# Kernel optimization log

Hardware: AMD Instinct MI355X
Metric: run time of the kernel (lower is better)

## Reference

```python
import jax, jax.numpy as jnp
import numpy as np

EPS = 1e-12

def gcn_layer(x, W, row, col, vals, n_nodes):
    # support = x @ W ; out = relu(spmm(adj, support)) with adj in COO form
    support = x @ W                                  # [N, out]
    msgs = vals[:, None] * support[col]              # [E, out] gather
    agg = jax.ops.segment_sum(msgs, row, num_segments=n_nodes)
    return jax.nn.relu(agg)

def l2norm(x):
    return x / jnp.maximum(jnp.linalg.norm(x, axis=1, keepdims=True), EPS)

def setup_inputs() -> dict:
    key = jax.random.key(0)
    ks = jax.random.split(key, 16)
    N, D, A, Da, E = 20000, 1000, 1000, 100, 160000
    inp = {
        'emb_sr': jax.random.normal(ks[0], (N, D), jnp.float32) * 0.02,
        'emb_tg': jax.random.normal(ks[1], (N, D), jnp.float32) * 0.02,
        'attr_weight_sr': jax.random.uniform(ks[2], (N, A), jnp.float32),
        'attr_weight_tg': jax.random.uniform(ks[3], (N, A), jnp.float32),
        'row_sr': jax.random.randint(ks[4], (E,), 0, N, jnp.int32),
        'col_sr': jax.random.randint(ks[5], (E,), 0, N, jnp.int32),
        'vals_sr': jax.random.uniform(ks[6], (E,), jnp.float32),
        'row_tg': jax.random.randint(ks[7], (E,), 0, N, jnp.int32),
        'col_tg': jax.random.randint(ks[8], (E,), 0, N, jnp.int32),
        'vals_tg': jax.random.uniform(ks[9], (E,), jnp.float32),
        'W_s0': jax.random.normal(ks[10], (D, D), jnp.float32) * (1.0 / np.sqrt(D)),
        'W_s1': jax.random.normal(ks[11], (D, D), jnp.float32) * (1.0 / np.sqrt(D)),
        'W_a11': jax.random.normal(ks[12], (A, Da), jnp.float32) * (1.0 / np.sqrt(A)),
        'W_a12': jax.random.normal(ks[13], (A, Da), jnp.float32) * (1.0 / np.sqrt(A)),
        'W_a2': jax.random.normal(ks[14], (Da, Da), jnp.float32) * (1.0 / np.sqrt(Da)),
    }
    return inp

def reference(emb_sr, emb_tg, attr_weight_sr, attr_weight_tg,
              row_sr, col_sr, vals_sr, row_tg, col_tg, vals_tg,
              W_s0, W_s1, W_a11, W_a12, W_a2):
    N = emb_sr.shape[0]
    M = emb_tg.shape[0]
    # structural branch: 2 shared GCN layers over each graph
    sr = emb_sr
    tg = emb_tg
    for W in (W_s0, W_s1):
        sr = gcn_layer(sr, W, row_sr, col_sr, vals_sr, N)
        tg = gcn_layer(tg, W, row_tg, col_tg, vals_tg, M)
    sr = l2norm(sr)
    tg = l2norm(tg)
    # attribute branch
    sr_a = gcn_layer(attr_weight_sr, W_a11, row_sr, col_sr, vals_sr, N)
    sr_a = gcn_layer(sr_a, W_a2, row_sr, col_sr, vals_sr, N)
    tg_a = gcn_layer(attr_weight_tg, W_a12, row_tg, col_tg, vals_tg, M)
    tg_a = gcn_layer(tg_a, W_a2, row_tg, col_tg, vals_tg, M)
    return (sr, tg, sr_a, tg_a)
```

## Files before the change

### kernel.cpp

```cpp
#include <hip/hip_runtime.h>

#define N_NODES 20000
#define D_IN    1000
#define E_EDGES 160000
#define DA      100

#define MP   20096
#define DP   1024
#define DAP  128
#define MBLK 157
#define PEMAX (E_EDGES + 4 * N_NODES)

typedef __bf16 bf16x8 __attribute__((ext_vector_type(8)));
typedef float  f32x4  __attribute__((ext_vector_type(4)));

__device__ __forceinline__ short f2bf(float f) {
  unsigned u = __float_as_uint(f);
  return (short)((u + 0x7FFFu + ((u >> 16) & 1u)) >> 16);
}
__device__ __forceinline__ float bf2f(short s) {
  return __uint_as_float(((unsigned)(unsigned short)s) << 16);
}

#define GLDS16(g, l) __builtin_amdgcn_global_load_lds( \
    (const __attribute__((address_space(1))) void*)(g), \
    (__attribute__((address_space(3))) void*)(l), 16, 0, 0)


__global__ void cvt_pad2_k(const float* __restrict__ s0, const float* __restrict__ s1,
                           int R, int C,
                           short* __restrict__ d0, short* __restrict__ d1, int Cp) {
  const float* src = blockIdx.z ? s1 : s0;
  short* dst = blockIdx.z ? d1 : d0;
  int r = blockIdx.y;
  int c0 = threadIdx.x * 4;
  short4 o = {0, 0, 0, 0};
  if (r < R) {
    if (c0 + 3 < C) {
      float4 v = *(const float4*)&src[(size_t)r * C + c0];
      o.x = f2bf(v.x); o.y = f2bf(v.y); o.z = f2bf(v.z); o.w = f2bf(v.w);
    } else {
#pragma unroll
      for (int j = 0; j < 4; ++j) {
        float v = (c0 + j < C) ? src[(size_t)r * C + c0 + j] : 0.f;
        ((short*)&o)[j] = f2bf(v);
      }
    }
  }
  *(short4*)&dst[(size_t)r * Cp + c0] = o;
}

__global__ void cvt_w_t2_k(const float* __restrict__ s0, const float* __restrict__ s1,
                           int K, int Nc,
                           short* __restrict__ d0, short* __restrict__ d1, int Kp) {
  const float* src = blockIdx.z ? s1 : s0;
  short* dst = blockIdx.z ? d1 : d0;
  int n = blockIdx.y;
  int k = blockIdx.x * blockDim.x + threadIdx.x;
  if (k >= Kp) return;
  float v = (k < K && n < Nc) ? src[(size_t)k * Nc + n] : 0.f;
  dst[(size_t)n * Kp + k] = f2bf(v);
}

__global__ void zero_int_k(int* p, int n) {
  int i = blockIdx.x * blockDim.x + threadIdx.x;
  if (i < n) p[i] = 0;
}


__global__ void hist2_k(const int* __restrict__ row0, const int* __restrict__ row1, int E,
                        int* __restrict__ deg0, int* __restrict__ deg1) {
  int e = blockIdx.x * blockDim.x + threadIdx.x;
  if (e < E) atomicAdd(&deg0[row0[e]], 1);
  else if (e < 2 * E) atomicAdd(&deg1[row1[e - E]], 1);
}

#define SCAN_T 1024
#define SCAN_C 20
__launch_bounds__(SCAN_T)
__global__ void scan_pad2_k(const int* __restrict__ dg0, const int* __restrict__ dg1, int n,
                            int* __restrict__ p0, int* __restrict__ p1) {
  const int* deg = blockIdx.x ? dg1 : dg0;
  int* poffs = blockIdx.x ? p1 : p0;
  __shared__ int lds[SCAN_T];
  int t = threadIdx.x;
  int base = t * SCAN_C;
  int v[SCAN_C];
  int s = 0;
#pragma unroll
  for (int i = 0; i < SCAN_C; ++i) {
    int idx = base + i;
    int x = (idx < n) ? ((deg[idx] + 3) & ~3) : 0;
    s += x;
    v[i] = s;
  }
  lds[t] = s;
  __syncthreads();
  for (int off = 1; off < SCAN_T; off <<= 1) {
    int add = (t >= off) ? lds[t - off] : 0;
    __syncthreads();
    lds[t] += add;
    __syncthreads();
  }
  int prefix = lds[t] - s;
#pragma unroll
  for (int i = 0; i < SCAN_C; ++i) {
    int idx = base + i;
    if (idx < n) poffs[idx + 1] = v[i] + prefix;
  }
  if (t == 0) poffs[0] = 0;
}

__global__ void scatter_pack2_k(const int* __restrict__ row0, const int* __restrict__ col0,
                                const float* __restrict__ val0,
                                const int* __restrict__ row1, const int* __restrict__ col1,
                                const float* __restrict__ val1, int E,
                                const int* __restrict__ po0, const int* __restrict__ po1,
                                int* __restrict__ cur0, int* __restrict__ cur1,
                                int2* __restrict__ pk0, int2* __restrict__ pk1) {
  int e = blockIdx.x * blockDim.x + threadIdx.x;
  if (e < E) {
    int r = row0[e];
    int p = atomicAdd(&cur0[r], 1);
    pk0[po0[r] + p] = make_int2(col0[e], __float_as_int(val0[e]));
  } else if (e < 2 * E) {
    int ee = e - E;
    int r = row1[ee];
    int p = atomicAdd(&cur1[r], 1);
    pk1[po1[r] + p] = make_int2(col1[ee], __float_as_int(val1[ee]));
  }
}

__launch_bounds__(256, 2)
__global__ void gemm_bf16_k(const short* __restrict__ A0, const short* __restrict__ A1, int lda,
                            const short* __restrict__ Bt0, const short* __restrict__ Bt1, int ldb,
                            short* __restrict__ C0, short* __restrict__ C1, int ldc, int K,
                            int nbCol, int nbRow) {
  __shared__ short As[128 * 64];
  __shared__ short Bs[128 * 64];

  int orig = blockIdx.x;
  int nwg = gridDim.x;
  int q = nwg >> 3, rr = nwg & 7;
  int xcd = orig & 7, idx = orig >> 3;
  int wg = (xcd < rr ? xcd * (q + 1) : rr * (q + 1) + (xcd - rr) * q) + idx;
  int colB = wg % nbCol;
  int t2   = wg / nbCol;
  int rowB = t2 % nbRow;
  int z    = t2 / nbRow;

  const short* A  = z ? A1 : A0;
  const short* Bt = z ? Bt1 : Bt0;
  short* C        = z ? C1 : C0;

  const int tid  = threadIdx.x;
  const int lane = tid & 63;
  const int wid  = tid >> 6;
  const int wr   = wid >> 1;
  const int wc   = wid & 1;
  const int rowBase = rowB * 128;
  const int colBase = colB * 128;

  const int lrow = lane >> 3;
  const int kofs = (lane & 7) * 8;

  f32x4 acc[4][4];
#pragma unroll
  for (int m = 0; m < 4; ++m)
#pragma unroll
    for (int n = 0; n < 4; ++n)
      acc[m][n] = (f32x4){0.f, 0.f, 0.f, 0.f};

  for (int k0 = 0; k0 < K; k0 += 64) {
#pragma unroll
    for (int c = 0; c < 4; ++c) {
      int chunk = wid * 4 + c;
      int r = chunk * 8 + lrow;
      const short* g = A + (size_t)(rowBase + r) * lda + k0 + kofs;
      GLDS16(g, &As[chunk * 8 * 64]);
    }
#pragma unroll
    for (int c = 0; c < 4; ++c) {
      int chunk = wid * 4 + c;
      int r = chunk * 8 + lrow;
      const short* g = Bt + (size_t)(colBase + r) * ldb + k0 + kofs;
      GLDS16(g, &Bs[chunk * 8 * 64]);
    }
    __syncthreads();

    bf16x8 af[2][4], bfr[2][4];
#pragma unroll
    for (int kk = 0; kk < 2; ++kk) {
#pragma unroll
      for (int i = 0; i < 4; ++i) {
        int ar = wr * 64 + i * 16 + (lane & 15);
        af[kk][i]  = *(const bf16x8*)&As[ar * 64 + kk * 32 + (lane >> 4) * 8];
        int br = wc * 64 + i * 16 + (lane & 15);
        bfr[kk][i] = *(const bf16x8*)&Bs[br * 64 + kk * 32 + (lane >> 4) * 8];
      }
    }
#pragma unroll
    for (int kk = 0; kk < 2; ++kk)
#pragma unroll
      for (int m = 0; m < 4; ++m)
#pragma unroll
        for (int n = 0; n < 4; ++n)
          acc[m][n] = __builtin_amdgcn_mfma_f32_16x16x32_bf16(
              af[kk][m], bfr[kk][n], acc[m][n], 0, 0, 0);
    __syncthreads();
  }

#pragma unroll
  for (int m = 0; m < 4; ++m) {
#pragma unroll
    for (int n = 0; n < 4; ++n) {
      int row0 = rowBase + wr * 64 + m * 16 + (lane >> 4) * 4;
      int col  = colBase + wc * 64 + n * 16 + (lane & 15);
#pragma unroll
      for (int reg = 0; reg < 4; ++reg)
        C[(size_t)(row0 + reg) * ldc + col] = f2bf(acc[m][n][reg]);
    }
  }
}

template<int TPB, int VEC, int RPB>
__launch_bounds__(TPB)
__global__ void spmm_relu_v3(const int* __restrict__ po0, const int* __restrict__ po1,
                             const int2* __restrict__ pk0, const int2* __restrict__ pk1,
                             const short* __restrict__ S0, const short* __restrict__ S1, int ldS,
                             short* __restrict__ oB0, short* __restrict__ oB1, int ldB,
                             float* __restrict__ oF0, float* __restrict__ oF1, int outCols) {
  typedef short sv __attribute__((ext_vector_type(VEC)));
  const int* poffs    = blockIdx.z ? po1 : po0;
  const int2* packed  = blockIdx.z ? pk1 : pk0;
  const short* S      = blockIdx.z ? S1 : S0;
  short* outB         = blockIdx.z ? oB1 : oB0;
  float* outF         = blockIdx.z ? oF1 : oF0;
  int c0 = threadIdx.x * VEC;

  int rEnd = blockIdx.x * RPB + RPB;
  for (int r = blockIdx.x * RPB; r < rEnd; ++r) {
    int e0 = poffs[r], e1 = poffs[r + 1];
    float acc[VEC];
#pragma unroll
    for (int j = 0; j < VEC; ++j) acc[j] = 0.f;

    for (int i = e0; i < e1; i += 4) {
      const int4* p4 = (const int4*)&packed[i];
      int4 a = p4[0];
      int4 b = p4[1];
      sv s0 = *(const sv*)&S[(size_t)a.x * ldS + c0];
      sv s1 = *(const sv*)&S[(size_t)a.z * ldS + c0];
      sv s2 = *(const sv*)&S[(size_t)b.x * ldS + c0];
      sv s3 = *(const sv*)&S[(size_t)b.z * ldS + c0];
      float v0 = __int_as_float(a.y);
      float v1 = __int_as_float(a.w);
      float v2 = __int_as_float(b.y);
      float v3 = __int_as_float(b.w);
#pragma unroll
      for (int j = 0; j < VEC; ++j) {
        acc[j] += v0 * bf2f(s0[j]);
        acc[j] += v1 * bf2f(s1[j]);
        acc[j] += v2 * bf2f(s2[j]);
        acc[j] += v3 * bf2f(s3[j]);
      }
    }

    if (outB) {
      sv o;
#pragma unroll
      for (int j = 0; j < VEC; ++j) o[j] = f2bf(fmaxf(acc[j], 0.f));
      *(sv*)&outB[(size_t)r * ldB + c0] = o;
    } else {
#pragma unroll
      for (int j = 0; j < VEC; ++j)
        if (c0 + j < outCols)
          outF[(size_t)r * outCols + c0 + j] = fmaxf(acc[j], 0.f);
    }
  }
}

__global__ void l2norm2_k(const short* __restrict__ H0, const short* __restrict__ H1, int ldH,
                          float* __restrict__ o0, float* __restrict__ o1, int cols) {
  const short* H = blockIdx.y ? H1 : H0;
  float* out = blockIdx.y ? o1 : o0;
  __shared__ float red[4];
  int r = blockIdx.x;
  int t = threadIdx.x;
  float s = 0.f;
  for (int c = t; c < ldH; c += 256) {
    float v = bf2f(H[(size_t)r * ldH + c]);
    s += v * v;
  }
  for (int off = 32; off >= 1; off >>= 1) s += __shfl_down(s, off, 64);
  if ((t & 63) == 0) red[t >> 6] = s;
  __syncthreads();
  float tot = red[0] + red[1] + red[2] + red[3];
  float inv = 1.f / fmaxf(sqrtf(tot), 1e-12f);
  for (int c = t; c < cols; c += 256)
    out[(size_t)r * cols + c] = bf2f(H[(size_t)r * ldH + c]) * inv;
}


extern "C" void kernel_launch(void* const* d_in, const int* in_sizes, int n_in,
                              void* d_out, int out_size, void* d_ws, size_t ws_size,
                              hipStream_t stream) {
  const float* emb_sr  = (const float*)d_in[0];
  const float* emb_tg  = (const float*)d_in[1];
  const float* attr_sr = (const float*)d_in[2];
  const float* attr_tg = (const float*)d_in[3];
  const int*   row_sr  = (const int*)d_in[4];
  const int*   col_sr  = (const int*)d_in[5];
  const float* vals_sr = (const float*)d_in[6];
  const int*   row_tg  = (const int*)d_in[7];
  const int*   col_tg  = (const int*)d_in[8];
  const float* vals_tg = (const float*)d_in[9];
  const float* W_s0    = (const float*)d_in[10];
  const float* W_s1    = (const float*)d_in[11];
  const float* W_a11   = (const float*)d_in[12];
  const float* W_a12   = (const float*)d_in[13];
  const float* W_a2    = (const float*)d_in[14];

  const int N = N_NODES, Dd = D_IN, E = E_EDGES;

  char* ws = (char*)d_ws;
  size_t off = 0;
  auto alloc = [&](size_t bytes) -> void* {
    void* p = ws + off;
    off += (bytes + 255) & ~(size_t)255;
    return p;
  };
  short* X0 = (short*)alloc((size_t)MP * DP * 2);
  short* X1 = (short*)alloc((size_t)MP * DP * 2);
  short* T0 = (short*)alloc((size_t)MP * DP * 2);
  short* T1 = (short*)alloc((size_t)MP * DP * 2);
  short* Ws0t  = (short*)alloc((size_t)DP * DP * 2);
  short* Ws1t  = (short*)alloc((size_t)DP * DP * 2);
  short* Wa11t = (short*)alloc((size_t)DAP * DP * 2);
  short* Wa12t = (short*)alloc((size_t)DAP * DP * 2);
  short* Wa2t  = (short*)alloc((size_t)DAP * DAP * 2);
  int*  ibuf    = (int*)alloc((size_t)4 * N * 4);
  int2* pack_sr = (int2*)alloc((size_t)PEMAX * 8);
  int2* pack_tg = (int2*)alloc((size_t)PEMAX * 8);
  int*  poffs_sr = (int*)alloc((size_t)(N + 1) * 4);
  int*  poffs_tg = (int*)alloc((size_t)(N + 1) * 4);
  if (off > ws_size) return;

  int* deg_sr = ibuf;
  int* cur_sr = ibuf + N;
  int* deg_tg = ibuf + 2 * N;
  int* cur_tg = ibuf + 3 * N;
  const int ZERO_N = 4 * N + 2 * (PEMAX * 2);

  float* out_sr  = (float*)d_out;
  float* out_tg  = out_sr + (size_t)N * Dd;
  float* out_sra = out_tg + (size_t)N * Dd;
  float* out_tga = out_sra + (size_t)N * DA;

  zero_int_k<<<dim3((ZERO_N + 255) / 256), 256, 0, stream>>>(ibuf, ZERO_N);
  hist2_k<<<dim3((2 * E + 255) / 256), 256, 0, stream>>>(row_sr, row_tg, E, deg_sr, deg_tg);
  scan_pad2_k<<<2, SCAN_T, 0, stream>>>(deg_sr, deg_tg, N, poffs_sr, poffs_tg);
  scatter_pack2_k<<<dim3((2 * E + 255) / 256), 256, 0, stream>>>(
      row_sr, col_sr, vals_sr, row_tg, col_tg, vals_tg, E,
      poffs_sr, poffs_tg, cur_sr, cur_tg, pack_sr, pack_tg);

  cvt_w_t2_k<<<dim3(DP / 256, DP, 2), 256, 0, stream>>>(W_s0, W_s1, Dd, Dd, Ws0t, Ws1t, DP);
  cvt_w_t2_k<<<dim3(DP / 256, DAP, 2), 256, 0, stream>>>(W_a11, W_a12, Dd, DA, Wa11t, Wa12t, DP);
  cvt_w_t2_k<<<dim3(1, DAP, 1), 256, 0, stream>>>(W_a2, W_a2, DA, DA, Wa2t, Wa2t, DAP);

  cvt_pad2_k<<<dim3(1, MP, 2), 256, 0, stream>>>(emb_sr, emb_tg, N, Dd, X0, X1, DP);
  gemm_bf16_k<<<dim3(8 * MBLK * 2), 256, 0, stream>>>(X0, X1, DP, Ws0t, Ws0t, DP,
                                                      T0, T1, DP, DP, 8, MBLK);
  spmm_relu_v3<128, 8, 4><<<dim3(N / 4, 1, 2), 128, 0, stream>>>(
      poffs_sr, poffs_tg, pack_sr, pack_tg, T0, T1, DP, X0, X1, DP, nullptr, nullptr, 0);
  gemm_bf16_k<<<dim3(8 * MBLK * 2), 256, 0, stream>>>(X0, X1, DP, Ws1t, Ws1t, DP,
                                                      T0, T1, DP, DP, 8, MBLK);
  spmm_relu_v3<128, 8, 4><<<dim3(N / 4, 1, 2), 128, 0, stream>>>(
      poffs_sr, poffs_tg, pack_sr, pack_tg, T0, T1, DP, X0, X1, DP, nullptr, nullptr, 0);
  l2norm2_k<<<dim3(N, 2), 256, 0, stream>>>(X0, X1, DP, out_sr, out_tg, Dd);

  cvt_pad2_k<<<dim3(1, MP, 2), 256, 0, stream>>>(attr_sr, attr_tg, N, Dd, X0, X1, DP);
  gemm_bf16_k<<<dim3(1 * MBLK * 2), 256, 0, stream>>>(X0, X1, DP, Wa11t, Wa12t, DP,
                                                      T0, T1, DP, DP, 1, MBLK);
  spmm_relu_v3<64, 2, 4><<<dim3(N / 4, 1, 2), 64, 0, stream>>>(
      poffs_sr, poffs_tg, pack_sr, pack_tg, T0, T1, DP, X0, X1, DP, nullptr, nullptr, 0);
  gemm_bf16_k<<<dim3(1 * MBLK * 2), 256, 0, stream>>>(X0, X1, DP, Wa2t, Wa2t, DAP,
                                                      T0, T1, DP, DAP, 1, MBLK);
  spmm_relu_v3<64, 2, 4><<<dim3(N / 4, 1, 2), 64, 0, stream>>>(
      poffs_sr, poffs_tg, pack_sr, pack_tg, T0, T1, DP, nullptr, nullptr, 0, out_sra, out_tga, DA);
}
```

Before: 721.3 us.

## Restructure SpMM into 16-row blocks with column chunks and compact attribute stride

Replaces the per-block row loop SpMM with a kernel where each 256-thread block handles 16 rows, each row served by 16 lanes loading 8 bf16 values, with column chunks of 128 interleaved across blocks. For the attribute branch, the intermediate buffers now use a 128-wide stride instead of 1024, which shrinks the gathered rows and improves cache locality. The float-to-bf16 conversion now uses a native cast. The attribute SpMM uses 8-wide vectors instead of 2-wide, which may give more uneven per-lane work on rows with irregular degree.

Result: faster. 636.2 us (-11.8%).

```diff
diff --git a/kernel.cpp b/kernel.cpp
--- a/kernel.cpp
+++ b/kernel.cpp
@@ -9,14 +9,16 @@
 #define DP   1024
 #define DAP  128
 #define MBLK 157
+#define NRB  1250
 #define PEMAX (E_EDGES + 4 * N_NODES)
 
 typedef __bf16 bf16x8 __attribute__((ext_vector_type(8)));
 typedef float  f32x4  __attribute__((ext_vector_type(4)));
+typedef short  short8v __attribute__((ext_vector_type(8)));
 
 __device__ __forceinline__ short f2bf(float f) {
-  unsigned u = __float_as_uint(f);
-  return (short)((u + 0x7FFFu + ((u >> 16) & 1u)) >> 16);
+  __bf16 h = (__bf16)f;
+  return *(short*)&h;
 }
 __device__ __forceinline__ float bf2f(short s) {
   return __uint_as_float(((unsigned)(unsigned short)s) << 16);
@@ -223,60 +225,74 @@
   }
 }
 
-template<int TPB, int VEC, int RPB>
-__launch_bounds__(TPB)
-__global__ void spmm_relu_v3(const int* __restrict__ po0, const int* __restrict__ po1,
-                             const int2* __restrict__ pk0, const int2* __restrict__ pk1,
-                             const short* __restrict__ S0, const short* __restrict__ S1, int ldS,
-                             short* __restrict__ oB0, short* __restrict__ oB1, int ldB,
-                             float* __restrict__ oF0, float* __restrict__ oF1, int outCols) {
-  typedef short sv __attribute__((ext_vector_type(VEC)));
-  const int* poffs    = blockIdx.z ? po1 : po0;
-  const int2* packed  = blockIdx.z ? pk1 : pk0;
-  const short* S      = blockIdx.z ? S1 : S0;
-  short* outB         = blockIdx.z ? oB1 : oB0;
-  float* outF         = blockIdx.z ? oF1 : oF0;
-  int c0 = threadIdx.x * VEC;
-
-  int rEnd = blockIdx.x * RPB + RPB;
-  for (int r = blockIdx.x * RPB; r < rEnd; ++r) {
-    int e0 = poffs[r], e1 = poffs[r + 1];
-    float acc[VEC];
-#pragma unroll
-    for (int j = 0; j < VEC; ++j) acc[j] = 0.f;
-
-    for (int i = e0; i < e1; i += 4) {
-      const int4* p4 = (const int4*)&packed[i];
-      int4 a = p4[0];
-      int4 b = p4[1];
-      sv s0 = *(const sv*)&S[(size_t)a.x * ldS + c0];
-      sv s1 = *(const sv*)&S[(size_t)a.z * ldS + c0];
-      sv s2 = *(const sv*)&S[(size_t)b.x * ldS + c0];
-      sv s3 = *(const sv*)&S[(size_t)b.z * ldS + c0];
-      float v0 = __int_as_float(a.y);
-      float v1 = __int_as_float(a.w);
-      float v2 = __int_as_float(b.y);
-      float v3 = __int_as_float(b.w);
-#pragma unroll
-      for (int j = 0; j < VEC; ++j) {
-        acc[j] += v0 * bf2f(s0[j]);
-        acc[j] += v1 * bf2f(s1[j]);
-        acc[j] += v2 * bf2f(s2[j]);
-        acc[j] += v3 * bf2f(s3[j]);
-      }
-    }
-
-    if (outB) {
-      sv o;
-#pragma unroll
-      for (int j = 0; j < VEC; ++j) o[j] = f2bf(fmaxf(acc[j], 0.f));
-      *(sv*)&outB[(size_t)r * ldB + c0] = o;
-    } else {
-#pragma unroll
-      for (int j = 0; j < VEC; ++j)
-        if (c0 + j < outCols)
-          outF[(size_t)r * outCols + c0 + j] = fmaxf(acc[j], 0.f);
-    }
+template<int NCHUNK, int MODE>
+__launch_bounds__(256)
+__global__ void spmm_v5(const int* __restrict__ po0, const int* __restrict__ po1,
+                        const int2* __restrict__ pk0, const int2* __restrict__ pk1,
+                        const short* __restrict__ S0, const short* __restrict__ S1, int ldS,
+                        short* __restrict__ oB0, short* __restrict__ oB1, int ldB,
+                        float* __restrict__ oF0, float* __restrict__ oF1, int outCols) {
+  int orig = blockIdx.x;
+  int chunk, graph, rowBlk;
+  if (NCHUNK == 8) {
+    chunk = orig & 7;
+    int idx = orig >> 3;
+    graph = idx / NRB;
+    rowBlk = idx - graph * NRB;
+  } else {
+    chunk = 0;
+    graph = orig / NRB;
+    rowBlk = orig - graph * NRB;
+  }
+  const int* poffs   = graph ? po1 : po0;
+  const int2* packed = graph ? pk1 : pk0;
+  const short* S     = graph ? S1 : S0;
+  short* outB        = graph ? oB1 : oB0;
+  float* outF        = graph ? oF1 : oF0;
+
+  const int lane16 = threadIdx.x & 15;
+  const int rowloc = threadIdx.x >> 4;
+  const int r  = rowBlk * 16 + rowloc;
+  const int c0 = chunk * 128 + lane16 * 8;
+
+  int e0 = poffs[r], e1 = poffs[r + 1];
+  float acc[8];
+#pragma unroll
+  for (int j = 0; j < 8; ++j) acc[j] = 0.f;
+
+  for (int i = e0; i < e1; i += 4) {
+    const int4* p4 = (const int4*)&packed[i];
+    int4 a = p4[0];
+    int4 b = p4[1];
+    short8v s0 = *(const short8v*)&S[(size_t)a.x * ldS + c0];
+    short8v s1 = *(const short8v*)&S[(size_t)a.z * ldS + c0];
+    short8v s2 = *(const short8v*)&S[(size_t)b.x * ldS + c0];
+    short8v s3 = *(const short8v*)&S[(size_t)b.z * ldS + c0];
+    float v0 = __int_as_float(a.y);
+    float v1 = __int_as_float(a.w);
+    float v2 = __int_as_float(b.y);
+    float v3 = __int_as_float(b.w);
+#pragma unroll
+    for (int j = 0; j < 8; ++j) {
+      acc[j] += v0 * bf2f(s0[j]);
+      acc[j] += v1 * bf2f(s1[j]);
+      acc[j] += v2 * bf2f(s2[j]);
+      acc[j] += v3 * bf2f(s3[j]);
+    }
+  }
+#pragma unroll
+  for (int j = 0; j < 8; ++j) acc[j] = fmaxf(acc[j], 0.f);
+
+  if (MODE == 0) {
+    short8v o;
+#pragma unroll
+    for (int j = 0; j < 8; ++j) o[j] = f2bf(acc[j]);
+    *(short8v*)&outB[(size_t)r * ldB + c0] = o;
+  } else {
+#pragma unroll
+    for (int j = 0; j < 8; ++j)
+      if (c0 + j < outCols)
+        outF[(size_t)r * outCols + c0 + j] = acc[j];
   }
 }
 
@@ -371,21 +387,21 @@
   cvt_pad2_k<<<dim3(1, MP, 2), 256, 0, stream>>>(emb_sr, emb_tg, N, Dd, X0, X1, DP);
   gemm_bf16_k<<<dim3(8 * MBLK * 2), 256, 0, stream>>>(X0, X1, DP, Ws0t, Ws0t, DP,
                                                       T0, T1, DP, DP, 8, MBLK);
-  spmm_relu_v3<128, 8, 4><<<dim3(N / 4, 1, 2), 128, 0, stream>>>(
+  spmm_v5<8, 0><<<dim3(8 * 2 * NRB), 256, 0, stream>>>(
       poffs_sr, poffs_tg, pack_sr, pack_tg, T0, T1, DP, X0, X1, DP, nullptr, nullptr, 0);
   gemm_bf16_k<<<dim3(8 * MBLK * 2), 256, 0, stream>>>(X0, X1, DP, Ws1t, Ws1t, DP,
                                                       T0, T1, DP, DP, 8, MBLK);
-  spmm_relu_v3<128, 8, 4><<<dim3(N / 4, 1, 2), 128, 0, stream>>>(
+  spmm_v5<8, 0><<<dim3(8 * 2 * NRB), 256, 0, stream>>>(
       poffs_sr, poffs_tg, pack_sr, pack_tg, T0, T1, DP, X0, X1, DP, nullptr, nullptr, 0);
   l2norm2_k<<<dim3(N, 2), 256, 0, stream>>>(X0, X1, DP, out_sr, out_tg, Dd);
 
   cvt_pad2_k<<<dim3(1, MP, 2), 256, 0, stream>>>(attr_sr, attr_tg, N, Dd, X0, X1, DP);
   gemm_bf16_k<<<dim3(1 * MBLK * 2), 256, 0, stream>>>(X0, X1, DP, Wa11t, Wa12t, DP,
-                                                      T0, T1, DP, DP, 1, MBLK);
-  spmm_relu_v3<64, 2, 4><<<dim3(N / 4, 1, 2), 64, 0, stream>>>(
-      poffs_sr, poffs_tg, pack_sr, pack_tg, T0, T1, DP, X0, X1, DP, nullptr, nullptr, 0);
-  gemm_bf16_k<<<dim3(1 * MBLK * 2), 256, 0, stream>>>(X0, X1, DP, Wa2t, Wa2t, DAP,
-                                                      T0, T1, DP, DAP, 1, MBLK);
-  spmm_relu_v3<64, 2, 4><<<dim3(N / 4, 1, 2), 64, 0, stream>>>(
-      poffs_sr, poffs_tg, pack_sr, pack_tg, T0, T1, DP, nullptr, nullptr, 0, out_sra, out_tga, DA);
-}
+                                                      T0, T1, DAP, DP, 1, MBLK);
+  spmm_v5<1, 0><<<dim3(2 * NRB), 256, 0, stream>>>(
+      poffs_sr, poffs_tg, pack_sr, pack_tg, T0, T1, DAP, X0, X1, DAP, nullptr, nullptr, 0);
+  gemm_bf16_k<<<dim3(1 * MBLK * 2), 256, 0, stream>>>(X0, X1, DAP, Wa2t, Wa2t, DAP,
+                                                      T0, T1, DAP, DAP, 1, MBLK);
+  spmm_v5<1, 1><<<dim3(2 * NRB), 256, 0, stream>>>(
+      poffs_sr, poffs_tg, pack_sr, pack_tg, T0, T1, DAP, nullptr, nullptr, 0, out_sra, out_tga, DA);
+}
```
